# Performance work log

Hardware: AMD Instinct MI355X
Metric: run time of the kernel (lower is better)

## Reference

```python
import jax, jax.numpy as jnp
import numpy as np
import math

DIM = 1024
NUMHEADS = 16
HEAD_DIM = DIM // NUMHEADS
B, N = 4, 1024


def setup_inputs() -> dict:
    key = jax.random.key(0)
    ks = jax.random.split(key, 12)
    x = jax.random.normal(ks[0], (B, N, DIM), dtype=jnp.float32)
    decaymask = jax.random.uniform(ks[1], (NUMHEADS, N, N), dtype=jnp.float32)
    s = 1.0 / math.sqrt(DIM)
    wq = jax.random.normal(ks[2], (DIM, DIM), dtype=jnp.float32) * s
    bq = jnp.zeros((DIM,), dtype=jnp.float32)
    wk = jax.random.normal(ks[3], (DIM, DIM), dtype=jnp.float32) * s
    bk = jnp.zeros((DIM,), dtype=jnp.float32)
    wv = jax.random.normal(ks[4], (DIM, DIM), dtype=jnp.float32) * s
    bv = jnp.zeros((DIM,), dtype=jnp.float32)
    wo = jax.random.normal(ks[5], (DIM, DIM), dtype=jnp.float32) * s
    bo = jnp.zeros((DIM,), dtype=jnp.float32)
    return {"x": x, "decaymask": decaymask, "wq": wq, "bq": bq, "wk": wk,
            "bk": bk, "wv": wv, "bv": bv, "wo": wo, "bo": bo}


def reference(x, decaymask, wq, bq, wk, bk, wv, bv, wo, bo):
    Bx, Nx, D = x.shape
    # projections (torch Linear: x @ W^T + b)
    q = x @ wq.T + bq
    k = x @ wk.T + bk
    v = x @ wv.T + bv
    # [B, H, N, Hd]
    q = q.reshape(Bx, Nx, NUMHEADS, HEAD_DIM).transpose(0, 2, 1, 3)
    k = k.reshape(Bx, Nx, NUMHEADS, HEAD_DIM).transpose(0, 2, 1, 3)
    v = v.reshape(Bx, Nx, NUMHEADS, HEAD_DIM).transpose(0, 2, 1, 3)
    scores = jnp.einsum('bhqd,bhkd->bhqk', q, k) / math.sqrt(HEAD_DIM)
    scores = scores * decaymask[None]  # multiplicative decay mask before softmax
    attn = jax.nn.softmax(scores, axis=-1)
    out = jnp.einsum('bhqk,bhkd->bhqd', attn, v)
    out = out.transpose(0, 2, 1, 3).reshape(Bx, Nx, D)
    return out @ wo.T + bo
```

## Files before the change

### kernel.cpp

```cpp
#include <hip/hip_runtime.h>
#include <hip/hip_bf16.h>
#include <math.h>

typedef __bf16 bf16;
typedef __bf16 bf16x8 __attribute__((ext_vector_type(8)));
typedef __bf16 bf16x4 __attribute__((ext_vector_type(4)));
typedef float f32x4 __attribute__((ext_vector_type(4)));
typedef unsigned short u16;
typedef u16 u16x8 __attribute__((ext_vector_type(8)));

#define SEQ 1024
#define DIMSZ 1024
#define NHEADS 16
#define HEADDIM 64
#define BATCH 4

#define QSCALE 0.180336880f

typedef __attribute__((address_space(1))) const unsigned char gas_u8;
typedef __attribute__((address_space(3))) unsigned char las_u8;
__device__ __forceinline__ void gload16(const void* g, void* l) {
    __builtin_amdgcn_global_load_lds((const gas_u8*)g, (las_u8*)l, 16, 0, 0);
}

__device__ __forceinline__ void cvt_store(const float4 v, bf16* dst, int e0, float scale) {
    int row = e0 >> 10, col = e0 & 1023;
    int col2 = (col & ~63) | (col & 7) | (((((col >> 3) & 7) ^ (row & 7))) << 3);
    bf16x4 o;
    o[0] = (bf16)(v.x * scale);
    o[1] = (bf16)(v.y * scale);
    o[2] = (bf16)(v.z * scale);
    o[3] = (bf16)(v.w * scale);
    *reinterpret_cast<bf16x4*>(&dst[(size_t)row * 1024 + col2]) = o;
}

__global__ void cvt_swz(const float4* __restrict__ src, bf16* __restrict__ dst,
                        int n4, float scale) {
    int i = blockIdx.x * blockDim.x + threadIdx.x;
    if (i >= n4) return;
    cvt_store(src[i], dst, i << 2, scale);
}

__global__ void cvt_weights(const float4* __restrict__ wq, const float4* __restrict__ wk,
                            const float4* __restrict__ wv, const float4* __restrict__ wo,
                            bf16* __restrict__ wqkvb, bf16* __restrict__ wob) {
    int i = blockIdx.x * blockDim.x + threadIdx.x;
    int mat = i >> 18, li = i & 262143;
    const float4* s = (mat == 0) ? wq : (mat == 1) ? wk : (mat == 2) ? wv : wo;
    bf16* d = (mat < 3) ? (wqkvb + (size_t)mat * 1024 * 1024) : wob;
    cvt_store(s[li], d, li << 2, (mat == 0) ? QSCALE : 1.f);
}

__device__ __forceinline__ bf16x8 fragswz(const bf16* base, int row, int kb) {
    return *reinterpret_cast<const bf16x8*>(
        reinterpret_cast<const char*>(base) + row * 128 + (kb ^ ((row & 7) << 4)));
}

#define LDT 72
__device__ __forceinline__ bf16x8 ldsfrag72(const bf16* base, int row0, int k0, int lane) {
    return *reinterpret_cast<const bf16x8*>(base + (row0 + (lane & 15)) * LDT + k0 + ((lane >> 4) << 3));
}

template <int WN, int OUT_F32>
__global__ __launch_bounds__(256) void gemm_glds(
    const bf16* __restrict__ A, const bf16* __restrict__ Bm,
    const float* __restrict__ b0, const float* __restrict__ b1, const float* __restrict__ b2,
    float s0, void* __restrict__ Cv, int M, int N, int K)
{
    __shared__ __align__(16) bf16 As[128 * 64];
    __shared__ __align__(16) bf16 Bs[WN * 32 * 64];

    const int BN = WN * 32;
    const int nbn = N / BN;
    const int wrk = (blockIdx.x & 7) * ((int)gridDim.x >> 3) + (blockIdx.x >> 3);
    const int bm = wrk / nbn, bn = wrk % nbn;
    const int m0 = bm << 7, n0 = bn * BN;
    const int tid = threadIdx.x, lane = tid & 63, wid = tid >> 6;
    const int wr = wid >> 1, wc = wid & 1;
    const int lq = lane & 15, g = lane >> 4;

    f32x4 acc[4][WN];
    #pragma unroll
    for (int m = 0; m < 4; ++m)
        #pragma unroll
        for (int n = 0; n < WN; ++n)
            acc[m][n] = (f32x4){0.f, 0.f, 0.f, 0.f};

    for (int kt = 0; kt < K; kt += 64) {
        #pragma unroll
        for (int i = 0; i < 4; ++i) {
            int rb = wid * 32 + i * 8;
            gload16(&A[(size_t)(m0 + rb + (lane >> 3)) * K + kt + ((lane & 7) << 3)],
                    &As[rb * 64]);
        }
        #pragma unroll
        for (int i = 0; i < WN; ++i) {
            int rb = wid * (WN * 8) + i * 8;
            gload16(&Bm[(size_t)(n0 + rb + (lane >> 3)) * K + kt + ((lane & 7) << 3)],
                    &Bs[rb * 64]);
        }
        __syncthreads();

        bf16x8 af[4][2], bfr[WN][2];
        #pragma unroll
        for (int m = 0; m < 4; ++m)
            #pragma unroll
            for (int h2 = 0; h2 < 2; ++h2)
                af[m][h2] = fragswz(As, wr * 64 + m * 16 + lq, h2 * 64 + g * 16);
        #pragma unroll
        for (int n = 0; n < WN; ++n)
            #pragma unroll
            for (int h2 = 0; h2 < 2; ++h2)
                bfr[n][h2] = fragswz(Bs, wc * (WN * 16) + n * 16 + lq, h2 * 64 + g * 16);

        __builtin_amdgcn_s_setprio(1);
        #pragma unroll
        for (int m = 0; m < 4; ++m)
            #pragma unroll
            for (int n = 0; n < WN; ++n)
                #pragma unroll
                for (int h2 = 0; h2 < 2; ++h2)
                    acc[m][n] = __builtin_amdgcn_mfma_f32_16x16x32_bf16(
                        af[m][h2], bfr[n][h2], acc[m][n], 0, 0, 0);
        __builtin_amdgcn_s_setprio(0);
        __syncthreads();
    }

    const int seg = n0 >> 10;
    const float* bp = (seg == 0) ? b0 : ((seg == 1) ? b1 : b2);
    const float bsc = (seg == 0) ? s0 : 1.f;

    #pragma unroll
    for (int m = 0; m < 4; ++m) {
        #pragma unroll
        for (int n = 0; n < WN; ++n) {
            int rbase = m0 + wr * 64 + m * 16 + (g << 2);
            int col = n0 + wc * (WN * 16) + n * 16 + lq;
            float bv = bp[col - (seg << 10)] * bsc;
            #pragma unroll
            for (int r = 0; r < 4; ++r) {
                float v = acc[m][n][r] + bv;
                if (OUT_F32)
                    ((float*)Cv)[(size_t)(rbase + r) * N + col] = v;
                else
                    ((bf16*)Cv)[(size_t)(rbase + r) * N + col] = (bf16)v;
            }
        }
    }
}

struct KVRegs { bf16x8 k0, k1; u16x8 v0, v1; };

__device__ __forceinline__ void issue_loads(KVRegs& r, const bf16* qkv, int brow,
                                            int koff, int voff, int tid) {
    const int rK = tid >> 3, o8 = (tid & 7) << 3;
    r.k0 = *reinterpret_cast<const bf16x8*>(&qkv[(size_t)(brow + rK) * 3072 + koff + o8]);
    r.k1 = *reinterpret_cast<const bf16x8*>(&qkv[(size_t)(brow + rK + 32) * 3072 + koff + o8]);
    const int rV = rK << 1;
    r.v0 = *reinterpret_cast<const u16x8*>(&qkv[(size_t)(brow + rV) * 3072 + voff + o8]);
    r.v1 = *reinterpret_cast<const u16x8*>(&qkv[(size_t)(brow + rV + 1) * 3072 + voff + o8]);
}

__device__ __forceinline__ void write_stage(const KVRegs& r, bf16* Kb, bf16* Vb, int tid) {
    const int rK = tid >> 3, o = tid & 7, o8 = o << 3;
    *reinterpret_cast<bf16x8*>(&Kb[rK * LDT + o8]) = r.k0;
    *reinterpret_cast<bf16x8*>(&Kb[(rK + 32) * LDT + o8]) = r.k1;
    const int rV = rK << 1;
    #pragma unroll
    for (int j = 0; j < 8; ++j) {
        int d = o8 + j;
        int byteo = (d * 144 + rV * 2) ^ (o << 4);
        unsigned int w = (unsigned int)r.v0[j] | ((unsigned int)r.v1[j] << 16);
        *reinterpret_cast<unsigned int*>(reinterpret_cast<char*>(Vb) + byteo) = w;
    }
}

__device__ __forceinline__ void compute_stage(
    const bf16* Kb, const bf16* Vb, bf16* Psw,
    const float4 (&mreg)[4], const bf16x8 (&aqb)[2],
    f32x4& lacc, f32x4 (&oacc)[4], int lane)
{
    const int lq = lane & 15, g = lane >> 4;
    f32x4 sacc[4];
    #pragma unroll
    for (int ct = 0; ct < 4; ++ct) sacc[ct] = (f32x4){0.f, 0.f, 0.f, 0.f};
    __builtin_amdgcn_s_setprio(1);
    #pragma unroll
    for (int ct = 0; ct < 4; ++ct)
        #pragma unroll
        for (int h2 = 0; h2 < 2; ++h2)
            sacc[ct] = __builtin_amdgcn_mfma_f32_16x16x32_bf16(
                ldsfrag72(Kb, ct * 16, h2 * 32, lane), aqb[h2], sacc[ct], 0, 0, 0);
    __builtin_amdgcn_s_setprio(0);

    #pragma unroll
    for (int ct = 0; ct < 4; ++ct) {
        float p0 = __builtin_exp2f(sacc[ct][0] * mreg[ct].x);
        float p1 = __builtin_exp2f(sacc[ct][1] * mreg[ct].y);
        float p2 = __builtin_exp2f(sacc[ct][2] * mreg[ct].z);
        float p3 = __builtin_exp2f(sacc[ct][3] * mreg[ct].w);
        lacc[0] += p0; lacc[1] += p1; lacc[2] += p2; lacc[3] += p3;
        bf16x4 pb;
        pb[0] = (bf16)p0; pb[1] = (bf16)p1; pb[2] = (bf16)p2; pb[3] = (bf16)p3;
        *reinterpret_cast<bf16x4*>(&Psw[lq * LDT + ct * 16 + (g << 2)]) = pb;
    }

    __builtin_amdgcn_s_setprio(1);
    #pragma unroll
    for (int ot = 0; ot < 4; ++ot) {
        #pragma unroll
        for (int h2 = 0; h2 < 2; ++h2) {
            int d = ot * 16 + lq;
            int byteo = (d * 144 + (h2 * 32 + g * 8) * 2) ^ (((d >> 3) & 7) << 4);
            bf16x8 vf = *reinterpret_cast<const bf16x8*>(
                reinterpret_cast<const char*>(Vb) + byteo);
            bf16x8 pf = *reinterpret_cast<const bf16x8*>(&Psw[lq * LDT + h2 * 32 + g * 8]);
            oacc[ot] = __builtin_amdgcn_mfma_f32_16x16x32_bf16(vf, pf, oacc[ot], 0, 0, 0);
        }
    }
    __builtin_amdgcn_s_setprio(0);
}

__global__ __launch_bounds__(256) void attn_kernel(
    const bf16* __restrict__ qkv, const float* __restrict__ mask, bf16* __restrict__ Og)
{
    __shared__ __align__(16) bf16 Kbuf[2][64 * LDT];
    __shared__ __align__(16) bf16 Vbuf[2][64 * LDT];
    __shared__ __align__(16) bf16 Ps[4][16 * LDT];

    const int bid = blockIdx.x;
    const int xcd = bid & 7, slot = bid >> 3;
    const int pg = xcd * 32 + (slot >> 1);
    const int bp = slot & 1;
    const int h = pg >> 4, qblk = pg & 15;

    const int tid = threadIdx.x, lane = tid & 63, wid = tid >> 6;
    const int lq = lane & 15, g = lane >> 4;
    const int q = (qblk << 6) + wid * 16 + lq;
    const int koff = 1024 + h * HEADDIM, voff = 2048 + h * HEADDIM, qoff = h * HEADDIM;
    const float* mh = mask + (size_t)h * SEQ * SEQ + (size_t)q * SEQ;

    bf16x8 aq[2][2];
    #pragma unroll
    for (int bi = 0; bi < 2; ++bi)
        #pragma unroll
        for (int h2 = 0; h2 < 2; ++h2)
            aq[bi][h2] = *reinterpret_cast<const bf16x8*>(
                &qkv[(size_t)((bp * 2 + bi) * SEQ + q) * 3072 + qoff + h2 * 32 + g * 8]);

    f32x4 lacc[2] = {};
    f32x4 oacc[2][4] = {};

    KVRegs s0, s1;
    issue_loads(s0, qkv, (bp * 2 + 0) * SEQ, koff, voff, tid);
    issue_loads(s1, qkv, (bp * 2 + 1) * SEQ, koff, voff, tid);
    float4 mregA[4], mregB[4];
    #pragma unroll
    for (int ct = 0; ct < 4; ++ct) {
        mregA[ct] = *reinterpret_cast<const float4*>(&mh[ct * 16 + (g << 2)]);
        mregB[ct] = *reinterpret_cast<const float4*>(&mh[64 + ct * 16 + (g << 2)]);
    }
    write_stage(s0, Kbuf[0], Vbuf[0], tid);
    __syncthreads();

    for (int t = 0; t < 16; ++t) {
        if (t < 15) issue_loads(s0, qkv, (bp * 2 + 0) * SEQ + (t + 1) * 64, koff, voff, tid);
        compute_stage(Kbuf[0], Vbuf[0], Ps[wid], mregA, aq[0], lacc[0], oacc[0], lane);
        write_stage(s1, Kbuf[1], Vbuf[1], tid);
        __syncthreads();

        if (t < 15) issue_loads(s1, qkv, (bp * 2 + 1) * SEQ + (t + 1) * 64, koff, voff, tid);
        compute_stage(Kbuf[1], Vbuf[1], Ps[wid], mregA, aq[1], lacc[1], oacc[1], lane);
        #pragma unroll
        for (int ct = 0; ct < 4; ++ct) mregA[ct] = mregB[ct];
        if (t < 14)
            #pragma unroll
            for (int ct = 0; ct < 4; ++ct)
                mregB[ct] = *reinterpret_cast<const float4*>(&mh[(t + 2) * 64 + ct * 16 + (g << 2)]);
        if (t < 15) write_stage(s0, Kbuf[0], Vbuf[0], tid);
        __syncthreads();
    }

    #pragma unroll
    for (int bi = 0; bi < 2; ++bi) {
        float lsum = lacc[bi][0] + lacc[bi][1] + lacc[bi][2] + lacc[bi][3];
        lsum += __shfl_xor(lsum, 16, 64);
        lsum += __shfl_xor(lsum, 32, 64);
        float inv = 1.f / lsum;
        #pragma unroll
        for (int ot = 0; ot < 4; ++ot) {
            bf16x4 o;
            o[0] = (bf16)(oacc[bi][ot][0] * inv);
            o[1] = (bf16)(oacc[bi][ot][1] * inv);
            o[2] = (bf16)(oacc[bi][ot][2] * inv);
            o[3] = (bf16)(oacc[bi][ot][3] * inv);
            int lcol = ot * 16 + (g << 2);
            int chunk = (lcol >> 3) ^ (q & 7);
            int col = h * HEADDIM + (chunk << 3) + (lcol & 7);
            *reinterpret_cast<bf16x4*>(
                &Og[(size_t)((bp * 2 + bi) * SEQ + q) * DIMSZ + col]) = o;
        }
    }
}

extern "C" void kernel_launch(void* const* d_in, const int* in_sizes, int n_in,
                              void* d_out, int out_size, void* d_ws, size_t ws_size,
                              hipStream_t stream) {
    const float* x    = (const float*)d_in[0];
    const float* mask = (const float*)d_in[1];
    const float* wq   = (const float*)d_in[2];
    const float* bq   = (const float*)d_in[3];
    const float* wk   = (const float*)d_in[4];
    const float* bk   = (const float*)d_in[5];
    const float* wv   = (const float*)d_in[6];
    const float* bv   = (const float*)d_in[7];
    const float* wo   = (const float*)d_in[8];
    const float* bo   = (const float*)d_in[9];
    float* out = (float*)d_out;

    const size_t MTOK = (size_t)BATCH * SEQ;
    char* ws = (char*)d_ws;
    bf16* xb    = (bf16*)ws; ws += MTOK * DIMSZ * 2;
    bf16* wqkvb = (bf16*)ws; ws += (size_t)3 * DIMSZ * DIMSZ * 2;
    bf16* wob   = (bf16*)ws; ws += (size_t)DIMSZ * DIMSZ * 2;
    bf16* qkv   = (bf16*)ws; ws += MTOK * 3 * DIMSZ * 2;
    bf16* aob   = (bf16*)ws; ws += MTOK * DIMSZ * 2;

    int n4x = (int)(MTOK * DIMSZ / 4);
    cvt_swz<<<(n4x + 255) / 256, 256, 0, stream>>>((const float4*)x, xb, n4x, 1.f);
    cvt_weights<<<(4 * 262144) / 256, 256, 0, stream>>>(
        (const float4*)wq, (const float4*)wk, (const float4*)wv, (const float4*)wo,
        wqkvb, wob);

    gemm_glds<4, 0><<<(MTOK / 128) * (3 * DIMSZ / 128), 256, 0, stream>>>(
        xb, wqkvb, bq, bk, bv, QSCALE, qkv, (int)MTOK, 3 * DIMSZ, DIMSZ);

    attn_kernel<<<512, 256, 0, stream>>>(qkv, mask, aob);

    gemm_glds<2, 1><<<(MTOK / 128) * (DIMSZ / 64), 256, 0, stream>>>(
        aob, wob, bo, bo, bo, 1.f, out, (int)MTOK, DIMSZ, DIMSZ);
}
```

Baseline: 110.9 us.

## Split attention key range across two blocks with atomic partial-sum combine

Splits each attention block's key range in half, doubling the grid to 1024 blocks. Each half accumulates unnormalised outputs and row sums into fp32 buffers with atomicAdd. A new combine kernel then normalises and writes the swizzled bf16 input for the output GEMM. The fp32 partial output lives in the final output buffer, which is memset first, and the LDS layouts change from padded 72-wide rows to XOR-swizzled 64-wide rows, with setprio removed. This is meant to raise occupancy and parallelism. The cost is atomic traffic, two memsets and an extra kernel launch, and softmax relies on no max subtraction so the halves can be summed directly.

```diff
diff --git a/kernel.cpp b/kernel.cpp
--- a/kernel.cpp
+++ b/kernel.cpp
@@ -56,11 +56,6 @@
         reinterpret_cast<const char*>(base) + row * 128 + (kb ^ ((row & 7) << 4)));
 }
 
-#define LDT 72
-__device__ __forceinline__ bf16x8 ldsfrag72(const bf16* base, int row0, int k0, int lane) {
-    return *reinterpret_cast<const bf16x8*>(base + (row0 + (lane & 15)) * LDT + k0 + ((lane >> 4) << 3));
-}
-
 template <int WN, int OUT_F32>
 __global__ __launch_bounds__(256) void gemm_glds(
     const bf16* __restrict__ A, const bf16* __restrict__ Bm,
@@ -162,16 +157,18 @@
 }
 
 __device__ __forceinline__ void write_stage(const KVRegs& r, bf16* Kb, bf16* Vb, int tid) {
-    const int rK = tid >> 3, o = tid & 7, o8 = o << 3;
-    *reinterpret_cast<bf16x8*>(&Kb[rK * LDT + o8]) = r.k0;
-    *reinterpret_cast<bf16x8*>(&Kb[(rK + 32) * LDT + o8]) = r.k1;
-    const int rV = rK << 1;
+    const int rK = tid >> 3, o = tid & 7;
+    char* kb = reinterpret_cast<char*>(Kb);
+    int kx = (o << 4) ^ ((rK & 7) << 4);
+    *reinterpret_cast<bf16x8*>(kb + rK * 128 + kx) = r.k0;
+    *reinterpret_cast<bf16x8*>(kb + (rK + 32) * 128 + kx) = r.k1;
+    char* vb = reinterpret_cast<char*>(Vb);
     #pragma unroll
     for (int j = 0; j < 8; ++j) {
-        int d = o8 + j;
-        int byteo = (d * 144 + rV * 2) ^ (o << 4);
+        int d = (o << 3) + j;
+        int byteo = d * 128 + ((rK << 2) ^ ((d & 7) << 4));
         unsigned int w = (unsigned int)r.v0[j] | ((unsigned int)r.v1[j] << 16);
-        *reinterpret_cast<unsigned int*>(reinterpret_cast<char*>(Vb) + byteo) = w;
+        *reinterpret_cast<unsigned int*>(vb + byteo) = w;
     }
 }
 
@@ -184,15 +181,15 @@
     f32x4 sacc[4];
     #pragma unroll
     for (int ct = 0; ct < 4; ++ct) sacc[ct] = (f32x4){0.f, 0.f, 0.f, 0.f};
-    __builtin_amdgcn_s_setprio(1);
     #pragma unroll
     for (int ct = 0; ct < 4; ++ct)
         #pragma unroll
         for (int h2 = 0; h2 < 2; ++h2)
             sacc[ct] = __builtin_amdgcn_mfma_f32_16x16x32_bf16(
-                ldsfrag72(Kb, ct * 16, h2 * 32, lane), aqb[h2], sacc[ct], 0, 0, 0);
-    __builtin_amdgcn_s_setprio(0);
-
+                fragswz(Kb, ct * 16 + lq, h2 * 64 + g * 16), aqb[h2], sacc[ct], 0, 0, 0);
+
+    char* pb8 = reinterpret_cast<char*>(Psw);
+    const int px = (lq & 7) << 4;
     #pragma unroll
     for (int ct = 0; ct < 4; ++ct) {
         float p0 = __builtin_exp2f(sacc[ct][0] * mreg[ct].x);
@@ -200,45 +197,46 @@
         float p2 = __builtin_exp2f(sacc[ct][2] * mreg[ct].z);
         float p3 = __builtin_exp2f(sacc[ct][3] * mreg[ct].w);
         lacc[0] += p0; lacc[1] += p1; lacc[2] += p2; lacc[3] += p3;
-        bf16x4 pb;
-        pb[0] = (bf16)p0; pb[1] = (bf16)p1; pb[2] = (bf16)p2; pb[3] = (bf16)p3;
-        *reinterpret_cast<bf16x4*>(&Psw[lq * LDT + ct * 16 + (g << 2)]) = pb;
-    }
-
-    __builtin_amdgcn_s_setprio(1);
+        bf16x4 pbv;
+        pbv[0] = (bf16)p0; pbv[1] = (bf16)p1; pbv[2] = (bf16)p2; pbv[3] = (bf16)p3;
+        *reinterpret_cast<bf16x4*>(pb8 + lq * 128 + (((ct << 5) + (g << 3)) ^ px)) = pbv;
+    }
+
+    const char* vb = reinterpret_cast<const char*>(Vb);
     #pragma unroll
     for (int ot = 0; ot < 4; ++ot) {
         #pragma unroll
         for (int h2 = 0; h2 < 2; ++h2) {
             int d = ot * 16 + lq;
-            int byteo = (d * 144 + (h2 * 32 + g * 8) * 2) ^ (((d >> 3) & 7) << 4);
-            bf16x8 vf = *reinterpret_cast<const bf16x8*>(
-                reinterpret_cast<const char*>(Vb) + byteo);
-            bf16x8 pf = *reinterpret_cast<const bf16x8*>(&Psw[lq * LDT + h2 * 32 + g * 8]);
+            int kb = h2 * 64 + g * 16;
+            bf16x8 vf = *reinterpret_cast<const bf16x8*>(vb + d * 128 + (kb ^ ((d & 7) << 4)));
+            bf16x8 pf = *reinterpret_cast<const bf16x8*>(pb8 + lq * 128 + (kb ^ px));
             oacc[ot] = __builtin_amdgcn_mfma_f32_16x16x32_bf16(vf, pf, oacc[ot], 0, 0, 0);
         }
     }
-    __builtin_amdgcn_s_setprio(0);
-}
-
-__global__ __launch_bounds__(256) void attn_kernel(
-    const bf16* __restrict__ qkv, const float* __restrict__ mask, bf16* __restrict__ Og)
+}
+
+__global__ __launch_bounds__(256, 4) void attn_kernel(
+    const bf16* __restrict__ qkv, const float* __restrict__ mask,
+    float* __restrict__ Osum, float* __restrict__ lpart)
 {
-    __shared__ __align__(16) bf16 Kbuf[2][64 * LDT];
-    __shared__ __align__(16) bf16 Vbuf[2][64 * LDT];
-    __shared__ __align__(16) bf16 Ps[4][16 * LDT];
+    __shared__ __align__(16) bf16 Kbuf[2][64 * 64];
+    __shared__ __align__(16) bf16 Vbuf[2][64 * 64];
+    __shared__ __align__(16) bf16 Ps[4][16 * 64];
 
     const int bid = blockIdx.x;
     const int xcd = bid & 7, slot = bid >> 3;
-    const int pg = xcd * 32 + (slot >> 1);
     const int bp = slot & 1;
+    const int khalf = (slot >> 1) & 1;
+    const int pg = xcd * 32 + (slot >> 2);
     const int h = pg >> 4, qblk = pg & 15;
 
     const int tid = threadIdx.x, lane = tid & 63, wid = tid >> 6;
     const int lq = lane & 15, g = lane >> 4;
     const int q = (qblk << 6) + wid * 16 + lq;
+    const int k0 = khalf << 9;
     const int koff = 1024 + h * HEADDIM, voff = 2048 + h * HEADDIM, qoff = h * HEADDIM;
-    const float* mh = mask + (size_t)h * SEQ * SEQ + (size_t)q * SEQ;
+    const float* mh = mask + (size_t)h * SEQ * SEQ + (size_t)q * SEQ + k0;
 
     bf16x8 aq[2][2];
     #pragma unroll
@@ -252,8 +250,8 @@
     f32x4 oacc[2][4] = {};
 
     KVRegs s0, s1;
-    issue_loads(s0, qkv, (bp * 2 + 0) * SEQ, koff, voff, tid);
-    issue_loads(s1, qkv, (bp * 2 + 1) * SEQ, koff, voff, tid);
+    issue_loads(s0, qkv, (bp * 2 + 0) * SEQ + k0, koff, voff, tid);
+    issue_loads(s1, qkv, (bp * 2 + 1) * SEQ + k0, koff, voff, tid);
     float4 mregA[4], mregB[4];
     #pragma unroll
     for (int ct = 0; ct < 4; ++ct) {
@@ -263,44 +261,54 @@
     write_stage(s0, Kbuf[0], Vbuf[0], tid);
     __syncthreads();
 
-    for (int t = 0; t < 16; ++t) {
-        if (t < 15) issue_loads(s0, qkv, (bp * 2 + 0) * SEQ + (t + 1) * 64, koff, voff, tid);
+    for (int t = 0; t < 8; ++t) {
+        if (t < 7) issue_loads(s0, qkv, (bp * 2 + 0) * SEQ + k0 + (t + 1) * 64, koff, voff, tid);
         compute_stage(Kbuf[0], Vbuf[0], Ps[wid], mregA, aq[0], lacc[0], oacc[0], lane);
         write_stage(s1, Kbuf[1], Vbuf[1], tid);
         __syncthreads();
 
-        if (t < 15) issue_loads(s1, qkv, (bp * 2 + 1) * SEQ + (t + 1) * 64, koff, voff, tid);
+        if (t < 7) issue_loads(s1, qkv, (bp * 2 + 1) * SEQ + k0 + (t + 1) * 64, koff, voff, tid);
         compute_stage(Kbuf[1], Vbuf[1], Ps[wid], mregA, aq[1], lacc[1], oacc[1], lane);
         #pragma unroll
         for (int ct = 0; ct < 4; ++ct) mregA[ct] = mregB[ct];
-        if (t < 14)
+        if (t < 6)
             #pragma unroll
             for (int ct = 0; ct < 4; ++ct)
                 mregB[ct] = *reinterpret_cast<const float4*>(&mh[(t + 2) * 64 + ct * 16 + (g << 2)]);
-        if (t < 15) write_stage(s0, Kbuf[0], Vbuf[0], tid);
+        if (t < 7) write_stage(s0, Kbuf[0], Vbuf[0], tid);
         __syncthreads();
     }
 
     #pragma unroll
     for (int bi = 0; bi < 2; ++bi) {
+        int row = (bp * 2 + bi) * SEQ + q;
         float lsum = lacc[bi][0] + lacc[bi][1] + lacc[bi][2] + lacc[bi][3];
         lsum += __shfl_xor(lsum, 16, 64);
         lsum += __shfl_xor(lsum, 32, 64);
-        float inv = 1.f / lsum;
+        if (g == 0) atomicAdd(&lpart[row * 16 + h], lsum);
         #pragma unroll
         for (int ot = 0; ot < 4; ++ot) {
-            bf16x4 o;
-            o[0] = (bf16)(oacc[bi][ot][0] * inv);
-            o[1] = (bf16)(oacc[bi][ot][1] * inv);
-            o[2] = (bf16)(oacc[bi][ot][2] * inv);
-            o[3] = (bf16)(oacc[bi][ot][3] * inv);
-            int lcol = ot * 16 + (g << 2);
-            int chunk = (lcol >> 3) ^ (q & 7);
-            int col = h * HEADDIM + (chunk << 3) + (lcol & 7);
-            *reinterpret_cast<bf16x4*>(
-                &Og[(size_t)((bp * 2 + bi) * SEQ + q) * DIMSZ + col]) = o;
-        }
-    }
+            float* dst = &Osum[(size_t)row * DIMSZ + h * HEADDIM + ot * 16 + (g << 2)];
+            #pragma unroll
+            for (int r = 0; r < 4; ++r)
+                atomicAdd(dst + r, oacc[bi][ot][r]);
+        }
+    }
+}
+
+__global__ __launch_bounds__(256) void combine_kernel(
+    const float* __restrict__ Osum, const float* __restrict__ lpart,
+    bf16* __restrict__ aob)
+{
+    int i = blockIdx.x * blockDim.x + threadIdx.x;
+    int row = i >> 8, c4 = (i & 255) << 2;
+    float4 o = *reinterpret_cast<const float4*>(&Osum[(size_t)row * 1024 + c4]);
+    float inv = 1.f / lpart[row * 16 + (c4 >> 6)];
+    int col2 = (c4 & ~63) | (c4 & 7) | (((((c4 >> 3) & 7) ^ (row & 7))) << 3);
+    bf16x4 ob;
+    ob[0] = (bf16)(o.x * inv); ob[1] = (bf16)(o.y * inv);
+    ob[2] = (bf16)(o.z * inv); ob[3] = (bf16)(o.w * inv);
+    *reinterpret_cast<bf16x4*>(&aob[(size_t)row * 1024 + col2]) = ob;
 }
 
 extern "C" void kernel_launch(void* const* d_in, const int* in_sizes, int n_in,
@@ -325,6 +333,10 @@
     bf16* wob   = (bf16*)ws; ws += (size_t)DIMSZ * DIMSZ * 2;
     bf16* qkv   = (bf16*)ws; ws += MTOK * 3 * DIMSZ * 2;
     bf16* aob   = (bf16*)ws; ws += MTOK * DIMSZ * 2;
+    float* lpart = (float*)ws; ws += MTOK * NHEADS * 4;
+
+    hipMemsetAsync(d_out, 0, MTOK * DIMSZ * 4, stream);
+    hipMemsetAsync(lpart, 0, MTOK * NHEADS * 4, stream);
 
     int n4x = (int)(MTOK * DIMSZ / 4);
     cvt_swz<<<(n4x + 255) / 256, 256, 0, stream>>>((const float4*)x, xb, n4x, 1.f);
@@ -335,7 +347,9 @@
     gemm_glds<4, 0><<<(MTOK / 128) * (3 * DIMSZ / 128), 256, 0, stream>>>(
         xb, wqkvb, bq, bk, bv, QSCALE, qkv, (int)MTOK, 3 * DIMSZ, DIMSZ);
 
-    attn_kernel<<<512, 256, 0, stream>>>(qkv, mask, aob);
+    attn_kernel<<<1024, 256, 0, stream>>>(qkv, mask, (float*)d_out, lpart);
+
+    combine_kernel<<<4096, 256, 0, stream>>>((const float*)d_out, lpart, aob);
 
     gemm_glds<2, 1><<<(MTOK / 128) * (DIMSZ / 64), 256, 0, stream>>>(
         aob, wob, bo, bo, bo, 1.f, out, (int)MTOK, DIMSZ, DIMSZ);
```

Measured after the change: 344.9 us. 3.11x slower.

## Widen attention KV tiles to 128 and stage K via direct global-to-LDS swizzled loads

Applied to the files above, without the earlier changes.

The attention kernel now processes 128-key tiles instead of 64, halving loop iterations and barriers per batch pair. K tiles are loaded straight into LDS with global_load_lds, which needs an XOR-swizzled layout; the QKV GEMM epilogue now writes its bf16 output pre-swizzled so those loads land conflict-free. V and P buffers move to swizzled 128-byte rows instead of padded ones, and the s_setprio hints are removed. The mask values for each tile are no longer prefetched a stage ahead, so their load latency may be exposed, and LDS use and register pressure grow with the larger tile.

```diff
diff --git a/kernel.cpp b/kernel.cpp
--- a/kernel.cpp
+++ b/kernel.cpp
@@ -14,6 +14,8 @@
 #define NHEADS 16
 #define HEADDIM 64
 #define BATCH 4
+#define MTOK (BATCH * SEQ)
+#define KT 128
 
 #define QSCALE 0.180336880f
 
@@ -56,11 +58,6 @@
         reinterpret_cast<const char*>(base) + row * 128 + (kb ^ ((row & 7) << 4)));
 }
 
-#define LDT 72
-__device__ __forceinline__ bf16x8 ldsfrag72(const bf16* base, int row0, int k0, int lane) {
-    return *reinterpret_cast<const bf16x8*>(base + (row0 + (lane & 15)) * LDT + k0 + ((lane >> 4) << 3));
-}
-
 template <int WN, int OUT_F32>
 __global__ __launch_bounds__(256) void gemm_glds(
     const bf16* __restrict__ A, const bf16* __restrict__ Bm,
@@ -113,7 +110,6 @@
             for (int h2 = 0; h2 < 2; ++h2)
                 bfr[n][h2] = fragswz(Bs, wc * (WN * 16) + n * 16 + lq, h2 * 64 + g * 16);
 
-        __builtin_amdgcn_s_setprio(1);
         #pragma unroll
         for (int m = 0; m < 4; ++m)
             #pragma unroll
@@ -122,7 +118,6 @@
                 for (int h2 = 0; h2 < 2; ++h2)
                     acc[m][n] = __builtin_amdgcn_mfma_f32_16x16x32_bf16(
                         af[m][h2], bfr[n][h2], acc[m][n], 0, 0, 0);
-        __builtin_amdgcn_s_setprio(0);
         __syncthreads();
     }
 
@@ -140,93 +135,120 @@
             #pragma unroll
             for (int r = 0; r < 4; ++r) {
                 float v = acc[m][n][r] + bv;
-                if (OUT_F32)
-                    ((float*)Cv)[(size_t)(rbase + r) * N + col] = v;
-                else
-                    ((bf16*)Cv)[(size_t)(rbase + r) * N + col] = (bf16)v;
+                int rr = rbase + r;
+                if (OUT_F32) {
+                    ((float*)Cv)[(size_t)rr * N + col] = v;
+                } else {
+                    int col2 = (col & ~63) | (col & 7) |
+                               ((((col >> 3) & 7) ^ (rr & 7)) << 3);
+                    ((bf16*)Cv)[(size_t)rr * N + col2] = (bf16)v;
+                }
             }
         }
     }
 }
 
-struct KVRegs { bf16x8 k0, k1; u16x8 v0, v1; };
-
-__device__ __forceinline__ void issue_loads(KVRegs& r, const bf16* qkv, int brow,
-                                            int koff, int voff, int tid) {
-    const int rK = tid >> 3, o8 = (tid & 7) << 3;
-    r.k0 = *reinterpret_cast<const bf16x8*>(&qkv[(size_t)(brow + rK) * 3072 + koff + o8]);
-    r.k1 = *reinterpret_cast<const bf16x8*>(&qkv[(size_t)(brow + rK + 32) * 3072 + koff + o8]);
-    const int rV = rK << 1;
-    r.v0 = *reinterpret_cast<const u16x8*>(&qkv[(size_t)(brow + rV) * 3072 + voff + o8]);
-    r.v1 = *reinterpret_cast<const u16x8*>(&qkv[(size_t)(brow + rV + 1) * 3072 + voff + o8]);
-}
-
-__device__ __forceinline__ void write_stage(const KVRegs& r, bf16* Kb, bf16* Vb, int tid) {
-    const int rK = tid >> 3, o = tid & 7, o8 = o << 3;
-    *reinterpret_cast<bf16x8*>(&Kb[rK * LDT + o8]) = r.k0;
-    *reinterpret_cast<bf16x8*>(&Kb[(rK + 32) * LDT + o8]) = r.k1;
-    const int rV = rK << 1;
-    #pragma unroll
-    for (int j = 0; j < 8; ++j) {
-        int d = o8 + j;
-        int byteo = (d * 144 + rV * 2) ^ (o << 4);
-        unsigned int w = (unsigned int)r.v0[j] | ((unsigned int)r.v1[j] << 16);
-        *reinterpret_cast<unsigned int*>(reinterpret_cast<char*>(Vb) + byteo) = w;
-    }
-}
-
-__device__ __forceinline__ void compute_stage(
-    const bf16* Kb, const bf16* Vb, bf16* Psw,
-    const float4 (&mreg)[4], const bf16x8 (&aqb)[2],
+struct VR { u16x8 v[4]; };
+
+__device__ __forceinline__ void vload(VR& r, const bf16* qkv, int grow0, int voff, int tid) {
+    const int kp = tid >> 3, o = tid & 7;
+    #pragma unroll
+    for (int p = 0; p < 2; ++p)
+        #pragma unroll
+        for (int e = 0; e < 2; ++e) {
+            int grow = grow0 + ((p * 32 + kp) << 1) + e;
+            int chunk = o ^ (grow & 7);
+            r.v[2 * p + e] = *reinterpret_cast<const u16x8*>(
+                &qkv[(size_t)grow * 3072 + voff + (chunk << 3)]);
+        }
+}
+
+__device__ __forceinline__ void write_v(const VR& r, bf16* Vb, int tid) {
+    const int kp = tid >> 3, o = tid & 7;
+    #pragma unroll
+    for (int p = 0; p < 2; ++p) {
+        char* vb = reinterpret_cast<char*>(Vb + p * 64 * 64);
+        #pragma unroll
+        for (int j = 0; j < 8; ++j) {
+            int d = (o << 3) + j;
+            int byteo = d * 128 + ((kp << 2) ^ ((d & 7) << 4));
+            unsigned int w = (unsigned int)r.v[2 * p][j] | ((unsigned int)r.v[2 * p + 1][j] << 16);
+            *reinterpret_cast<unsigned int*>(vb + byteo) = w;
+        }
+    }
+}
+
+__device__ __forceinline__ void kstage(const bf16* qkv, int grow0, int koff,
+                                       bf16* Kb, int wid, int lane) {
+    #pragma unroll
+    for (int p = 0; p < 4; ++p) {
+        int rb = wid * 32 + p * 8;
+        gload16(&qkv[(size_t)(grow0 + rb + (lane >> 3)) * 3072 + koff + ((lane & 7) << 3)],
+                &Kb[rb * 64]);
+    }
+}
+
+__device__ __forceinline__ void compute_tile(
+    const bf16* Kb, const bf16* Vb, bf16* Pw,
+    const float4 (&mreg)[8], const bf16x8 (&aqb)[2],
     f32x4& lacc, f32x4 (&oacc)[4], int lane)
 {
     const int lq = lane & 15, g = lane >> 4;
-    f32x4 sacc[4];
-    #pragma unroll
-    for (int ct = 0; ct < 4; ++ct) sacc[ct] = (f32x4){0.f, 0.f, 0.f, 0.f};
-    __builtin_amdgcn_s_setprio(1);
-    #pragma unroll
-    for (int ct = 0; ct < 4; ++ct)
+    f32x4 sacc[8];
+    #pragma unroll
+    for (int ct = 0; ct < 8; ++ct) sacc[ct] = (f32x4){0.f, 0.f, 0.f, 0.f};
+    #pragma unroll
+    for (int ct = 0; ct < 8; ++ct)
         #pragma unroll
         for (int h2 = 0; h2 < 2; ++h2)
             sacc[ct] = __builtin_amdgcn_mfma_f32_16x16x32_bf16(
-                ldsfrag72(Kb, ct * 16, h2 * 32, lane), aqb[h2], sacc[ct], 0, 0, 0);
-    __builtin_amdgcn_s_setprio(0);
-
-    #pragma unroll
-    for (int ct = 0; ct < 4; ++ct) {
-        float p0 = __builtin_exp2f(sacc[ct][0] * mreg[ct].x);
-        float p1 = __builtin_exp2f(sacc[ct][1] * mreg[ct].y);
-        float p2 = __builtin_exp2f(sacc[ct][2] * mreg[ct].z);
-        float p3 = __builtin_exp2f(sacc[ct][3] * mreg[ct].w);
-        lacc[0] += p0; lacc[1] += p1; lacc[2] += p2; lacc[3] += p3;
-        bf16x4 pb;
-        pb[0] = (bf16)p0; pb[1] = (bf16)p1; pb[2] = (bf16)p2; pb[3] = (bf16)p3;
-        *reinterpret_cast<bf16x4*>(&Psw[lq * LDT + ct * 16 + (g << 2)]) = pb;
-    }
-
-    __builtin_amdgcn_s_setprio(1);
-    #pragma unroll
-    for (int ot = 0; ot < 4; ++ot) {
-        #pragma unroll
-        for (int h2 = 0; h2 < 2; ++h2) {
-            int d = ot * 16 + lq;
-            int byteo = (d * 144 + (h2 * 32 + g * 8) * 2) ^ (((d >> 3) & 7) << 4);
-            bf16x8 vf = *reinterpret_cast<const bf16x8*>(
-                reinterpret_cast<const char*>(Vb) + byteo);
-            bf16x8 pf = *reinterpret_cast<const bf16x8*>(&Psw[lq * LDT + h2 * 32 + g * 8]);
-            oacc[ot] = __builtin_amdgcn_mfma_f32_16x16x32_bf16(vf, pf, oacc[ot], 0, 0, 0);
-        }
-    }
-    __builtin_amdgcn_s_setprio(0);
+                fragswz(Kb, ct * 16 + lq, h2 * 64 + g * 16), aqb[h2], sacc[ct], 0, 0, 0);
+
+    const int px = (lq & 7) << 4;
+    #pragma unroll
+    for (int s = 0; s < 2; ++s) {
+        char* pb8 = reinterpret_cast<char*>(Pw + s * 16 * 64);
+        #pragma unroll
+        for (int c = 0; c < 4; ++c) {
+            int ct = s * 4 + c;
+            float p0 = __builtin_exp2f(sacc[ct][0] * mreg[ct].x);
+            float p1 = __builtin_exp2f(sacc[ct][1] * mreg[ct].y);
+            float p2 = __builtin_exp2f(sacc[ct][2] * mreg[ct].z);
+            float p3 = __builtin_exp2f(sacc[ct][3] * mreg[ct].w);
+            lacc[0] += p0; lacc[1] += p1; lacc[2] += p2; lacc[3] += p3;
+            bf16x4 pbv;
+            pbv[0] = (bf16)p0; pbv[1] = (bf16)p1; pbv[2] = (bf16)p2; pbv[3] = (bf16)p3;
+            *reinterpret_cast<bf16x4*>(pb8 + lq * 128 + (((c << 5) + (g << 3)) ^ px)) = pbv;
+        }
+    }
+
+    #pragma unroll
+    for (int s = 0; s < 2; ++s) {
+        const char* vb = reinterpret_cast<const char*>(Vb + s * 64 * 64);
+        const char* pb8 = reinterpret_cast<const char*>(Pw + s * 16 * 64);
+        bf16x8 pf[2];
+        #pragma unroll
+        for (int h2 = 0; h2 < 2; ++h2)
+            pf[h2] = *reinterpret_cast<const bf16x8*>(pb8 + lq * 128 + ((h2 * 64 + g * 16) ^ px));
+        #pragma unroll
+        for (int ot = 0; ot < 4; ++ot) {
+            #pragma unroll
+            for (int h2 = 0; h2 < 2; ++h2) {
+                int d = ot * 16 + lq;
+                int kb = h2 * 64 + g * 16;
+                bf16x8 vf = *reinterpret_cast<const bf16x8*>(vb + d * 128 + (kb ^ ((d & 7) << 4)));
+                oacc[ot] = __builtin_amdgcn_mfma_f32_16x16x32_bf16(vf, pf[h2], oacc[ot], 0, 0, 0);
+            }
+        }
+    }
 }
 
 __global__ __launch_bounds__(256) void attn_kernel(
     const bf16* __restrict__ qkv, const float* __restrict__ mask, bf16* __restrict__ Og)
 {
-    __shared__ __align__(16) bf16 Kbuf[2][64 * LDT];
-    __shared__ __align__(16) bf16 Vbuf[2][64 * LDT];
-    __shared__ __align__(16) bf16 Ps[4][16 * LDT];
+    __shared__ __align__(16) bf16 Kbuf[2][KT * 64];
+    __shared__ __align__(16) bf16 Vbuf[2][2][64 * 64];
+    __shared__ __align__(16) bf16 Ps[4][2][16 * 64];
 
     const int bid = blockIdx.x;
     const int xcd = bid & 7, slot = bid >> 3;
@@ -238,46 +260,51 @@
     const int lq = lane & 15, g = lane >> 4;
     const int q = (qblk << 6) + wid * 16 + lq;
     const int koff = 1024 + h * HEADDIM, voff = 2048 + h * HEADDIM, qoff = h * HEADDIM;
+    const int b0 = bp * 2, b1 = bp * 2 + 1;
     const float* mh = mask + (size_t)h * SEQ * SEQ + (size_t)q * SEQ;
 
     bf16x8 aq[2][2];
     #pragma unroll
     for (int bi = 0; bi < 2; ++bi)
         #pragma unroll
-        for (int h2 = 0; h2 < 2; ++h2)
+        for (int h2 = 0; h2 < 2; ++h2) {
+            int chunk = (h2 * 4 + g) ^ (q & 7);
             aq[bi][h2] = *reinterpret_cast<const bf16x8*>(
-                &qkv[(size_t)((bp * 2 + bi) * SEQ + q) * 3072 + qoff + h2 * 32 + g * 8]);
+                &qkv[(size_t)((b0 + bi) * SEQ + q) * 3072 + qoff + (chunk << 3)]);
+        }
 
     f32x4 lacc[2] = {};
     f32x4 oacc[2][4] = {};
 
-    KVRegs s0, s1;
-    issue_loads(s0, qkv, (bp * 2 + 0) * SEQ, koff, voff, tid);
-    issue_loads(s1, qkv, (bp * 2 + 1) * SEQ, koff, voff, tid);
-    float4 mregA[4], mregB[4];
-    #pragma unroll
-    for (int ct = 0; ct < 4; ++ct) {
-        mregA[ct] = *reinterpret_cast<const float4*>(&mh[ct * 16 + (g << 2)]);
-        mregB[ct] = *reinterpret_cast<const float4*>(&mh[64 + ct * 16 + (g << 2)]);
-    }
-    write_stage(s0, Kbuf[0], Vbuf[0], tid);
+    kstage(qkv, b0 * SEQ, koff, Kbuf[0], wid, lane);
+    kstage(qkv, b1 * SEQ, koff, Kbuf[1], wid, lane);
+    VR s0, s1;
+    vload(s0, qkv, b0 * SEQ, voff, tid);
+    vload(s1, qkv, b1 * SEQ, voff, tid);
+    write_v(s0, Vbuf[0][0], tid);
+    write_v(s1, Vbuf[1][0], tid);
     __syncthreads();
 
-    for (int t = 0; t < 16; ++t) {
-        if (t < 15) issue_loads(s0, qkv, (bp * 2 + 0) * SEQ + (t + 1) * 64, koff, voff, tid);
-        compute_stage(Kbuf[0], Vbuf[0], Ps[wid], mregA, aq[0], lacc[0], oacc[0], lane);
-        write_stage(s1, Kbuf[1], Vbuf[1], tid);
+    for (int t = 0; t < 8; ++t) {
+        float4 mreg[8];
+        #pragma unroll
+        for (int ct = 0; ct < 8; ++ct)
+            mreg[ct] = *reinterpret_cast<const float4*>(&mh[t * KT + ct * 16 + (g << 2)]);
+
+        if (t >= 1) {
+            kstage(qkv, b1 * SEQ + t * KT, koff, Kbuf[1], wid, lane);
+            write_v(s1, Vbuf[1][0], tid);
+        }
+        if (t < 7) vload(s0, qkv, b0 * SEQ + (t + 1) * KT, voff, tid);
+        compute_tile(Kbuf[0], Vbuf[0][0], Ps[wid][0], mreg, aq[0], lacc[0], oacc[0], lane);
         __syncthreads();
 
-        if (t < 15) issue_loads(s1, qkv, (bp * 2 + 1) * SEQ + (t + 1) * 64, koff, voff, tid);
-        compute_stage(Kbuf[1], Vbuf[1], Ps[wid], mregA, aq[1], lacc[1], oacc[1], lane);
-        #pragma unroll
-        for (int ct = 0; ct < 4; ++ct) mregA[ct] = mregB[ct];
-        if (t < 14)
-            #pragma unroll
-            for (int ct = 0; ct < 4; ++ct)
-                mregB[ct] = *reinterpret_cast<const float4*>(&mh[(t + 2) * 64 + ct * 16 + (g << 2)]);
-        if (t < 15) write_stage(s0, Kbuf[0], Vbuf[0], tid);
+        if (t < 7) {
+            kstage(qkv, b0 * SEQ + (t + 1) * KT, koff, Kbuf[0], wid, lane);
+            vload(s1, qkv, b1 * SEQ + (t + 1) * KT, voff, tid);
+            write_v(s0, Vbuf[0][0], tid);
+        }
+        compute_tile(Kbuf[1], Vbuf[1][0], Ps[wid][0], mreg, aq[1], lacc[1], oacc[1], lane);
         __syncthreads();
     }
 
@@ -298,7 +325,7 @@
             int chunk = (lcol >> 3) ^ (q & 7);
             int col = h * HEADDIM + (chunk << 3) + (lcol & 7);
             *reinterpret_cast<bf16x4*>(
-                &Og[(size_t)((bp * 2 + bi) * SEQ + q) * DIMSZ + col]) = o;
+                &Og[(size_t)((b0 + bi) * SEQ + q) * DIMSZ + col]) = o;
         }
     }
 }
@@ -318,25 +345,24 @@
     const float* bo   = (const float*)d_in[9];
     float* out = (float*)d_out;
 
-    const size_t MTOK = (size_t)BATCH * SEQ;
     char* ws = (char*)d_ws;
-    bf16* xb    = (bf16*)ws; ws += MTOK * DIMSZ * 2;
+    bf16* xb    = (bf16*)ws; ws += (size_t)MTOK * DIMSZ * 2;
     bf16* wqkvb = (bf16*)ws; ws += (size_t)3 * DIMSZ * DIMSZ * 2;
     bf16* wob   = (bf16*)ws; ws += (size_t)DIMSZ * DIMSZ * 2;
-    bf16* qkv   = (bf16*)ws; ws += MTOK * 3 * DIMSZ * 2;
-    bf16* aob   = (bf16*)ws; ws += MTOK * DIMSZ * 2;
-
-    int n4x = (int)(MTOK * DIMSZ / 4);
+    bf16* qkv   = (bf16*)ws; ws += (size_t)MTOK * 3 * DIMSZ * 2;
+    bf16* aob   = (bf16*)ws; ws += (size_t)MTOK * DIMSZ * 2;
+
+    int n4x = (int)((size_t)MTOK * DIMSZ / 4);
     cvt_swz<<<(n4x + 255) / 256, 256, 0, stream>>>((const float4*)x, xb, n4x, 1.f);
     cvt_weights<<<(4 * 262144) / 256, 256, 0, stream>>>(
         (const float4*)wq, (const float4*)wk, (const float4*)wv, (const float4*)wo,
         wqkvb, wob);
 
     gemm_glds<4, 0><<<(MTOK / 128) * (3 * DIMSZ / 128), 256, 0, stream>>>(
-        xb, wqkvb, bq, bk, bv, QSCALE, qkv, (int)MTOK, 3 * DIMSZ, DIMSZ);
+        xb, wqkvb, bq, bk, bv, QSCALE, qkv, MTOK, 3 * DIMSZ, DIMSZ);
 
     attn_kernel<<<512, 256, 0, stream>>>(qkv, mask, aob);
 
     gemm_glds<2, 1><<<(MTOK / 128) * (DIMSZ / 64), 256, 0, stream>>>(
-        aob, wob, bo, bo, bo, 1.f, out, (int)MTOK, DIMSZ, DIMSZ);
-}
+        aob, wob, bo, bo, bo, 1.f, out, MTOK, DIMSZ, DIMSZ);
+}
```

Measured after the change: 138.6 us. +25.1%, slower.
